# Optimization experiments

Hardware: AMD Instinct MI355X
Metric: run time of the kernel (lower is better)

Reference implementation:

```python
import jax, jax.numpy as jnp
import numpy as np

B, C, IMG, P, E, H, F, L, NC = 32, 1, 224, 16, 256, 16, 3072, 12, 8
NP_ = (IMG // P) ** 2          # 196 patches
S = NP_ + 1                    # 197 tokens (cls + patches)
HD = E // H                    # 16 head dim
DVL, DVR, DVT = NP_ // 4 + 1, NP_ // 4, NP_ // 4   # 50, 49, 49 -> sum + DVT = 197


def _ln(x, g, b, eps=1e-5):
    m = x.mean(-1, keepdims=True)
    v = ((x - m) ** 2).mean(-1, keepdims=True)
    return (x - m) / jnp.sqrt(v + eps) * g + b


def setup_inputs():
    key = jax.random.key(0)
    ks = iter(jax.random.split(key, 64))
    def w(shape, s=0.02):
        return jax.random.normal(next(ks), shape, jnp.float32) * s
    return dict(
        x=jax.random.normal(next(ks), (B, C, IMG, IMG), jnp.float32),
        W_patch=w((E, C, P, P)), b_patch=jnp.zeros((E,), jnp.float32),
        cls_tok=w((1, 1, E), 1.0), pos_emb=w((1, S, E), 1.0),
        Wkl=w((E, E)), bkl=jnp.zeros((E,), jnp.float32),
        Wvl=w((DVL, E)), bvl=jnp.zeros((DVL,), jnp.float32),
        Wkr=w((E, E)), bkr=jnp.zeros((E,), jnp.float32),
        Wvr=w((DVR, E)), bvr=jnp.zeros((DVR,), jnp.float32),
        Wkt=w((E, E)), bkt=jnp.zeros((E,), jnp.float32),
        Wvt=w((DVT, E)), bvt=jnp.zeros((DVT,), jnp.float32),
        ln1_g=jnp.ones((L, E), jnp.float32), ln1_b=jnp.zeros((L, E), jnp.float32),
        Wqkv=w((L, 3 * E, E)), bqkv=jnp.zeros((L, 3 * E), jnp.float32),
        Wo=w((L, E, E)), bo=jnp.zeros((L, E), jnp.float32),
        ln2_g=jnp.ones((L, E), jnp.float32), ln2_b=jnp.zeros((L, E), jnp.float32),
        W1=w((L, F, E)), b1=jnp.zeros((L, F), jnp.float32),
        W2=w((L, E, F)), b2=jnp.zeros((L, E), jnp.float32),
        lnf_g=jnp.ones((E,), jnp.float32), lnf_b=jnp.zeros((E,), jnp.float32),
        W_head=w((NC, E)), b_head=jnp.zeros((NC,), jnp.float32),
    )


def reference(x, W_patch, b_patch, cls_tok, pos_emb,
              Wkl, bkl, Wvl, bvl, Wkr, bkr, Wvr, bvr, Wkt, bkt, Wvt, bvt,
              ln1_g, ln1_b, Wqkv, bqkv, Wo, bo, ln2_g, ln2_b, W1, b1, W2, b2,
              lnf_g, lnf_b, W_head, b_head):
    Bsz = x.shape[0]
    scale_k = 1.0 / jnp.sqrt(jnp.float32(E))
    # patch embedding: conv with stride == kernel == patch size
    h = jax.lax.conv_general_dilated(x, W_patch, (P, P), 'VALID',
                                     dimension_numbers=('NCHW', 'OIHW', 'NCHW'))
    h = h + b_patch[None, :, None, None]                   # (B, E, 14, 14)
    h = h.reshape(Bsz, E, NP_).transpose(0, 2, 1)          # (B, 196, E)
    h = jnp.concatenate([jnp.broadcast_to(cls_tok, (Bsz, 1, E)), h], 1) + pos_emb

    # linear rotatory attention fusing each sample with its batch neighbors
    def rag(xl, xt, xr):                                   # each (S, E)
        rt = xt.mean(0)                                    # target summary (E,)
        al = jax.nn.softmax((xl @ Wkl.T + bkl) @ rt * scale_k)
        rl = al @ (xl @ Wvl.T + bvl)                       # (DVL,)
        ar = jax.nn.softmax((xr @ Wkr.T + bkr) @ rt * scale_k)
        rr = ar @ (xr @ Wvr.T + bvr)                       # (DVR,)
        kt = xt @ Wkt.T + bkt
        vt = xt @ Wvt.T + bvt
        rtl = jax.nn.softmax(kt @ xl.mean(0) * scale_k) @ vt   # (DVT,)
        rtr = jax.nn.softmax(kt @ xr.mean(0) * scale_k) @ vt   # (DVT,)
        f = jnp.concatenate([rl, rtl, rtr, rr])            # (S,) = 50+49+49+49
        return jnp.outer(f, rt)                            # (S, E)

    mid = jax.vmap(rag)(h[:-2], h[1:-1], h[2:])            # (B-2, S, E) batched (no per-sample loop)
    h = jnp.concatenate([h[:1], mid, h[-1:]], 0)

    # standard pre-LN transformer encoder, scanned over stacked layer params
    def block(carry, p):
        g1, b1n, wqkv, bq, wo, bo_, g2, b2n, w1, bb1, w2, bb2 = p
        xn = _ln(carry, g1, b1n)
        qkv = xn @ wqkv.T + bq                             # (B, S, 3E)
        q, k, v = jnp.split(qkv, 3, axis=-1)
        q = q.reshape(Bsz, S, H, HD)
        k = k.reshape(Bsz, S, H, HD)
        v = v.reshape(Bsz, S, H, HD)
        att = jnp.einsum('bqhd,bkhd->bhqk', q, k) / jnp.sqrt(jnp.float32(HD))
        att = jax.nn.softmax(att, axis=-1)
        o = jnp.einsum('bhqk,bkhd->bqhd', att, v).reshape(Bsz, S, E)
        carry = carry + o @ wo.T + bo_
        xn2 = _ln(carry, g2, b2n)
        ff = jax.nn.gelu(xn2 @ w1.T + bb1, approximate=False) @ w2.T + bb2
        return carry + ff, None

    h, _ = jax.lax.scan(block, h, (ln1_g, ln1_b, Wqkv, bqkv, Wo, bo,
                                   ln2_g, ln2_b, W1, b1, W2, b2))
    cls = _ln(h[:, 0], lnf_g, lnf_b)
    return cls @ W_head.T + b_head
```

## Files before the change

kernel.cpp:

```cpp
#include <hip/hip_runtime.h>
#include <hip/hip_bf16.h>
#include <math.h>

constexpr int Bz  = 32;
constexpr int S   = 197;
constexpr int E   = 256;
constexpr int Hn  = 16;
constexpr int HD  = 16;
constexpr int Fd  = 3072;
constexpr int Ln  = 12;
constexpr int MS  = Bz * S;
constexpr int MP  = 6400;
constexpr int NPAT = 6272;
constexpr int DVL = 50, DVR = 49, DVT = 49;
constexpr size_t WLSTRIDE = 1835008;

typedef __attribute__((ext_vector_type(8))) short short8;
typedef __attribute__((ext_vector_type(4))) short short4v;
typedef __attribute__((ext_vector_type(4))) float f32x4;

__device__ __forceinline__ unsigned short f2bf(float f) {
    unsigned int u = __float_as_uint(f);
    u = (u + 0x7FFFu + ((u >> 16) & 1u)) >> 16;
    return (unsigned short)u;
}

__device__ __forceinline__ void gload_lds16(const void* g, void* l) {
    __builtin_amdgcn_global_load_lds(
        (const __attribute__((address_space(1))) void*)g,
        (__attribute__((address_space(3))) void*)l, 16, 0, 0);
}

__device__ __forceinline__ float wave_reduce(float v, int op) {
    #pragma unroll
    for (int off = 32; off > 0; off >>= 1) {
        float o = __shfl_xor(v, off, 64);
        v = op ? fmaxf(v, o) : v + o;
    }
    return v;
}

__device__ __forceinline__ float block_reduce(float v, float* red4, int op) {
    v = wave_reduce(v, op);
    int w = threadIdx.x >> 6;
    if ((threadIdx.x & 63) == 0) red4[w] = v;
    __syncthreads();
    float r = op ? fmaxf(fmaxf(red4[0], red4[1]), fmaxf(red4[2], red4[3]))
                 : (red4[0] + red4[1] + red4[2] + red4[3]);
    __syncthreads();
    return r;
}

__global__ __launch_bounds__(256) void patchify_kernel(
        const float* __restrict__ x, unsigned short* __restrict__ Ab) {
    int pi = blockIdx.x;
    int b = pi / 196, q = pi % 196;
    int i = q / 14, j = q % 14;
    int e = threadIdx.x, pr = e >> 4, pc = e & 15;
    float v = x[((size_t)(b * 224 + i * 16 + pr)) * 224 + j * 16 + pc];
    Ab[(size_t)pi * 256 + e] = f2bf(v);
}

__global__ __launch_bounds__(256) void cls_pos_kernel(
        const float* __restrict__ cls, const float* __restrict__ pos,
        float* __restrict__ h0) {
    int b = blockIdx.x, e = threadIdx.x;
    h0[(size_t)(b * S) * E + e] = cls[e] + pos[e];
}

__global__ __launch_bounds__(256) void convert_kernel(
        const float* __restrict__ src, unsigned short* __restrict__ dst) {
    int i4 = (blockIdx.x * 256 + threadIdx.x) * 4;
    float4 v = *(const float4*)(src + i4);
    ushort4 o;
    o.x = f2bf(v.x); o.y = f2bf(v.y); o.z = f2bf(v.z); o.w = f2bf(v.w);
    *(ushort4*)(dst + i4) = o;
}

__global__ __launch_bounds__(256) void convert_w_all_kernel(
        const float* __restrict__ wqkv, const float* __restrict__ wo,
        const float* __restrict__ w1, const float* __restrict__ w2,
        unsigned short* __restrict__ out) {
    size_t idx = (size_t)blockIdx.x * 256 + threadIdx.x;
    int l = (int)(idx / 458752);
    int r4 = (int)(idx % 458752) * 4;
    const float* src;
    if (r4 < 196608)       src = wqkv + (size_t)l * 196608 + r4;
    else if (r4 < 262144)  src = wo   + (size_t)l * 65536  + (r4 - 196608);
    else if (r4 < 1048576) src = w1   + (size_t)l * 786432 + (r4 - 262144);
    else                   src = w2   + (size_t)l * 786432 + (r4 - 1048576);
    float4 v = *(const float4*)src;
    ushort4 o;
    o.x = f2bf(v.x); o.y = f2bf(v.y); o.z = f2bf(v.z); o.w = f2bf(v.w);
    *(ushort4*)(out + (size_t)l * WLSTRIDE + r4) = o;
}

__global__ __launch_bounds__(256) void means_kernel(
        const float* __restrict__ h0, float* __restrict__ M) {
    int b = blockIdx.x, e = threadIdx.x;
    float s = 0.f;
    for (int t = 0; t < S; t++) s += h0[((size_t)(b * S + t)) * E + e];
    M[b * E + e] = s * (1.f / (float)S);
}

__global__ __launch_bounds__(256) void uvec_kernel(
        const float* __restrict__ M,
        const float* __restrict__ Wkl, const float* __restrict__ bkl,
        const float* __restrict__ Wkr, const float* __restrict__ bkr,
        const float* __restrict__ Wkt, const float* __restrict__ bkt,
        float* __restrict__ Ul, float* __restrict__ Ur, float* __restrict__ Ut,
        float* __restrict__ cl, float* __restrict__ cr, float* __restrict__ ct) {
    __shared__ float red4[4];
    int t = blockIdx.x, e = threadIdx.x;
    const float* mt = M + t * E;
    float a0 = 0.f, a1 = 0.f, a2 = 0.f;
    for (int i = 0; i < 256; i++) {
        float mi = mt[i];
        a0 += Wkl[(size_t)i * 256 + e] * mi;
        a1 += Wkr[(size_t)i * 256 + e] * mi;
        a2 += Wkt[(size_t)i * 256 + e] * mi;
    }
    Ul[t * E + e] = a0; Ur[t * E + e] = a1; Ut[t * E + e] = a2;
    float me = mt[e];
    float c0 = block_reduce(bkl[e] * me, red4, 0);
    float c1 = block_reduce(bkr[e] * me, red4, 0);
    float c2 = block_reduce(bkt[e] * me, red4, 0);
    if (e == 0) { cl[t] = c0; cr[t] = c1; ct[t] = c2; }
}

__global__ __launch_bounds__(256) void rag_score_kernel(
        const float* __restrict__ h0, const float* __restrict__ M,
        const float* __restrict__ Ul, const float* __restrict__ Ur,
        const float* __restrict__ Ut,
        const float* __restrict__ cl, const float* __restrict__ cr,
        const float* __restrict__ ct,
        const float* __restrict__ Wvl, const float* __restrict__ bvl,
        const float* __restrict__ Wvr, const float* __restrict__ bvr,
        const float* __restrict__ Wvt, const float* __restrict__ bvt,
        float* __restrict__ fbuf) {
    int t = blockIdx.x >> 2, br = blockIdx.x & 3;
    const float* xsrc; const float* u; float c;
    const float* Wv; const float* bv; int dv, fo;
    if (br == 0)      { xsrc = h0 + (size_t)t * S * E;       u = Ul + (t+1)*E; c = cl[t+1]; Wv = Wvl; bv = bvl; dv = DVL; fo = 0; }
    else if (br == 1) { xsrc = h0 + (size_t)(t+1) * S * E;   u = Ut + t*E;     c = ct[t];   Wv = Wvt; bv = bvt; dv = DVT; fo = DVL; }
    else if (br == 2) { xsrc = h0 + (size_t)(t+1) * S * E;   u = Ut + (t+2)*E; c = ct[t+2]; Wv = Wvt; bv = bvt; dv = DVT; fo = DVL + DVT; }
    else              { xsrc = h0 + (size_t)(t+2) * S * E;   u = Ur + (t+1)*E; c = cr[t+1]; Wv = Wvr; bv = bvr; dv = DVR; fo = DVL + 2*DVT; }
    __shared__ float us[256], sc[200], xbar[256], red4[4];
    int tid = threadIdx.x, w = tid >> 6, lane = tid & 63;
    us[tid] = u[tid];
    __syncthreads();
    float4 u4 = *(float4*)&us[lane * 4];
    for (int s = w; s < S; s += 4) {
        float4 x4 = *(const float4*)&xsrc[(size_t)s * E + lane * 4];
        float p = x4.x*u4.x + x4.y*u4.y + x4.z*u4.z + x4.w*u4.w;
        p = wave_reduce(p, 0);
        if (lane == 0) sc[s] = (p + c) * 0.0625f;
    }
    __syncthreads();
    float v = (tid < S) ? sc[tid] : -1e30f;
    float mx = block_reduce(v, red4, 1);
    float ex = (tid < S) ? expf(v - mx) : 0.f;
    float dn = block_reduce(ex, red4, 0);
    if (tid < S) sc[tid] = ex / dn;
    __syncthreads();
    float xb = 0.f;
    for (int s = 0; s < S; s++) xb += sc[s] * xsrc[(size_t)s * E + tid];
    xbar[tid] = xb;
    __syncthreads();
    float4 xb4 = *(float4*)&xbar[lane * 4];
    for (int d = w; d < dv; d += 4) {
        float4 w4 = *(const float4*)&Wv[(size_t)d * E + lane * 4];
        float p = w4.x*xb4.x + w4.y*xb4.y + w4.z*xb4.z + w4.w*xb4.w;
        p = wave_reduce(p, 0);
        if (lane == 0) fbuf[t * 256 + fo + d] = p + bv[d];
    }
}

__global__ __launch_bounds__(256) void rag_outer_kernel(
        const float* __restrict__ fbuf, const float* __restrict__ M,
        float* __restrict__ h1) {
    int bid = blockIdx.x;
    int t = bid / S, s = bid % S;
    float f = fbuf[t * 256 + s];
    int e = threadIdx.x;
    h1[((size_t)((t + 1) * S + s)) * E + e] = f * M[(t + 1) * E + e];
}

__global__ __launch_bounds__(256) void copy_edges(const float* __restrict__ h0,
                                                  float* __restrict__ h1) {
    int i = blockIdx.x * 256 + threadIdx.x;
    int n = S * E;
    if (i < n) h1[i] = h0[i];
    else if (i < 2 * n) {
        int j = i - n;
        size_t o = (size_t)31 * S * E + j;
        h1[o] = h0[o];
    }
}

__global__ __launch_bounds__(256) void ln_kernel(const float* __restrict__ in,
                                                 unsigned short* __restrict__ out,
                                                 const float* __restrict__ g,
                                                 const float* __restrict__ b) {
    int w = threadIdx.x >> 6, lane = threadIdx.x & 63;
    int tok = blockIdx.x * 4 + w;
    const float* row = in + (size_t)tok * E;
    float4 v = *(const float4*)&row[lane * 4];
    float mean = wave_reduce(v.x + v.y + v.z + v.w, 0) * (1.f / 256.f);
    float dx = v.x - mean, dy = v.y - mean, dz = v.z - mean, dw = v.w - mean;
    float var = wave_reduce(dx*dx + dy*dy + dz*dz + dw*dw, 0) * (1.f / 256.f);
    float inv = rsqrtf(var + 1e-5f);
    float4 gg = *(const float4*)&g[lane * 4];
    float4 bb = *(const float4*)&b[lane * 4];
    ushort4 o;
    o.x = f2bf(dx * inv * gg.x + bb.x);
    o.y = f2bf(dy * inv * gg.y + bb.y);
    o.z = f2bf(dz * inv * gg.z + bb.z);
    o.w = f2bf(dw * inv * gg.w + bb.w);
    *(ushort4*)&out[(size_t)tok * E + lane * 4] = o;
}

template <int MODE>
__global__ __launch_bounds__(256) void gemm_s64(
        const unsigned short* __restrict__ A, int lda,
        const unsigned short* __restrict__ W, int ldw,
        const float* __restrict__ bias,
        void* __restrict__ Cv, int ldc, int K, int MT, int NT,
        const float* __restrict__ pos) {
    __shared__ unsigned short As[2 * 64 * 64];
    __shared__ unsigned short Bs[2 * 64 * 64];
    const int id = blockIdx.x;
    const int mt = (id & 7) + 8 * (id / (8 * NT));
    const int nt = (id >> 3) % NT;
    if (mt >= MT) return;
    const int m0 = mt * 64, n0 = nt * 64;
    const int tid = threadIdx.x, wave = tid >> 6, lane = tid & 63;
    const int lr = lane & 15, kg = lane >> 4;
    const int srow = wave * 16 + (lane >> 3);
    const int scol = ((lane & 7) ^ (lane >> 3)) * 8;
    auto stage = [&](int bb, int k0) {
        #pragma unroll
        for (int q = 0; q < 2; q++) {
            gload_lds16(&A[(size_t)(m0 + srow + q * 8) * lda + k0 + scol],
                        &As[bb * 4096 + (wave * 16 + q * 8) * 64]);
            gload_lds16(&W[(size_t)(n0 + srow + q * 8) * ldw + k0 + scol],
                        &Bs[bb * 4096 + (wave * 16 + q * 8) * 64]);
        }
    };
    const int nIter = K >> 6;
    stage(0, 0);
    f32x4 acc[4] = {};
    for (int i = 0; i < nIter; i++) {
        __syncthreads();
        if (i + 1 < nIter) stage((i + 1) & 1, (i + 1) * 64);
        const int bb = i & 1;
        #pragma unroll
        for (int h = 0; h < 2; h++) {
            const int sw = ((h * 4 + kg) ^ (lr & 7)) * 8;
            short8 af = *(short8*)&As[bb * 4096 + (wave * 16 + lr) * 64 + sw];
            #pragma unroll
            for (int j = 0; j < 4; j++) {
                short8 bf = *(short8*)&Bs[bb * 4096 + (j * 16 + lr) * 64 + sw];
                acc[j] = __builtin_amdgcn_mfma_f32_16x16x32_bf16(af, bf, acc[j], 0, 0, 0);
            }
        }
    }
    #pragma unroll
    for (int j = 0; j < 4; j++) {
        int n = n0 + j * 16 + lr;
        float bv = bias ? bias[n] : 0.f;
        #pragma unroll
        for (int r = 0; r < 4; r++) {
            int m = m0 + wave * 16 + kg * 4 + r;
            float v = acc[j][r] + bv;
            if (MODE == 1) ((float*)Cv)[(size_t)m * ldc + n] += v;
            if (MODE == 2) {
                v = 0.5f * v * (1.f + erff(v * 0.70710678118654752f));
                ((unsigned short*)Cv)[(size_t)m * ldc + n] = f2bf(v);
            }
            if (MODE == 3) {
                int b = m / 196, s = m - b * 196 + 1;
                ((float*)Cv)[((size_t)(b * S + s)) * E + n] = v + pos[(size_t)s * E + n];
            }
            if (MODE == 4) ((unsigned short*)Cv)[(size_t)m * ldc + n] = f2bf(v);
        }
    }
}

static inline int s64_grid(int MT, int NT) { return ((MT + 7) / 8) * 8 * NT; }

__global__ __launch_bounds__(256) void attn_kernel(
        const unsigned short* __restrict__ qkv, unsigned short* __restrict__ o) {
    int b = blockIdx.x >> 4, hh = blockIdx.x & 15;
    __shared__ unsigned short Qs[208][32];
    __shared__ unsigned short Ks[208][32];
    __shared__ unsigned short Vt[16][224];
    __shared__ unsigned short Ps[4][16][224];
    int tid = threadIdx.x, wave = tid >> 6, lane = tid & 63;
    int lr = lane & 15, kg = lane >> 4;
    short8 z8 = {};
    if (tid < 208) {
        if (tid < 197) {
            size_t row = (size_t)(b * S + tid) * 768 + hh * 16;
            *(short8*)&Qs[tid][0] = *(const short8*)&qkv[row];
            *(short8*)&Qs[tid][8] = *(const short8*)&qkv[row + 8];
            *(short8*)&Ks[tid][0] = *(const short8*)&qkv[row + 256];
            *(short8*)&Ks[tid][8] = *(const short8*)&qkv[row + 264];
            union { short8 v8[2]; unsigned short u[16]; } vv;
            vv.v8[0] = *(const short8*)&qkv[row + 512];
            vv.v8[1] = *(const short8*)&qkv[row + 520];
            #pragma unroll
            for (int d = 0; d < 16; d++) Vt[d][tid] = vv.u[d];
        } else {
            *(short8*)&Qs[tid][0] = z8; *(short8*)&Qs[tid][8] = z8;
            *(short8*)&Ks[tid][0] = z8; *(short8*)&Ks[tid][8] = z8;
            #pragma unroll
            for (int d = 0; d < 16; d++) Vt[d][tid] = 0;
        }
        *(short8*)&Qs[tid][16] = z8; *(short8*)&Qs[tid][24] = z8;
        *(short8*)&Ks[tid][16] = z8; *(short8*)&Ks[tid][24] = z8;
    } else if (tid < 224) {
        #pragma unroll
        for (int d = 0; d < 16; d++) Vt[d][tid] = 0;
    }
    {
        short4v z4 = {};
        *(short4v*)&Ps[wave][lane >> 2][208 + (lane & 3) * 4] = z4;
    }
    __syncthreads();
    const f32x4 zf = {0.f, 0.f, 0.f, 0.f};
    for (int it = wave; it < 13; it += 4) {
        short8 qa = *(short8*)&Qs[it * 16 + lr][kg * 8];
        f32x4 sc[13];
        #pragma unroll
        for (int j = 0; j < 13; j++) {
            short8 kb = *(short8*)&Ks[j * 16 + lr][kg * 8];
            sc[j] = __builtin_amdgcn_mfma_f32_16x16x32_bf16(qa, kb, zf, 0, 0, 0);
        }
        float m[4] = {-1e30f, -1e30f, -1e30f, -1e30f};
        #pragma unroll
        for (int j = 0; j < 13; j++) {
            if (j * 16 + lr < 197) {
                #pragma unroll
                for (int r = 0; r < 4; r++) m[r] = fmaxf(m[r], sc[j][r]);
            }
        }
        #pragma unroll
        for (int off = 1; off < 16; off <<= 1)
            #pragma unroll
            for (int r = 0; r < 4; r++) m[r] = fmaxf(m[r], __shfl_xor(m[r], off, 64));
        float l[4] = {0.f, 0.f, 0.f, 0.f};
        #pragma unroll
        for (int j = 0; j < 13; j++) {
            bool valid = (j * 16 + lr) < 197;
            #pragma unroll
            for (int r = 0; r < 4; r++) {
                float p = valid ? __expf((sc[j][r] - m[r]) * 0.25f) : 0.f;
                l[r] += p;
                Ps[wave][kg * 4 + r][j * 16 + lr] = f2bf(p);
            }
        }
        #pragma unroll
        for (int off = 1; off < 16; off <<= 1)
            #pragma unroll
            for (int r = 0; r < 4; r++) l[r] += __shfl_xor(l[r], off, 64);
        f32x4 oa = zf;
        #pragma unroll
        for (int k0 = 0; k0 < 224; k0 += 32) {
            short8 pa = *(short8*)&Ps[wave][lr][k0 + kg * 8];
            short8 vb = *(short8*)&Vt[lr][k0 + kg * 8];
            oa = __builtin_amdgcn_mfma_f32_16x16x32_bf16(pa, vb, oa, 0, 0, 0);
        }
        #pragma unroll
        for (int r = 0; r < 4; r++) {
            int q = it * 16 + kg * 4 + r;
            if (q < 197)
                o[((size_t)(b * S + q)) * 256 + hh * 16 + lr] = f2bf(oa[r] / l[r]);
        }
    }
}

__global__ __launch_bounds__(256) void head_kernel(
        const float* __restrict__ h, const float* __restrict__ g,
        const float* __restrict__ bb, const float* __restrict__ Wh,
        const float* __restrict__ bh, float* __restrict__ out) {
    __shared__ float red4[4];
    __shared__ float xs[256];
    int b = blockIdx.x, e = threadIdx.x;
    float v = h[((size_t)(b * S)) * E + e];
    float mean = block_reduce(v, red4, 0) * (1.f / 256.f);
    float d = v - mean;
    float var = block_reduce(d * d, red4, 0) * (1.f / 256.f);
    float xn = d * rsqrtf(var + 1e-5f) * g[e] + bb[e];
    xs[e] = xn;
    __syncthreads();
    for (int n = 0; n < 8; n++) {
        float s = block_reduce(xs[e] * Wh[(size_t)n * 256 + e], red4, 0);
        if (e == 0) out[b * 8 + n] = s + bh[n];
    }
}

extern "C" void kernel_launch(void* const* d_in, const int* in_sizes, int n_in,
                              void* d_out, int out_size, void* d_ws, size_t ws_size,
                              hipStream_t stream) {
    const float* x      = (const float*)d_in[0];
    const float* W_patch= (const float*)d_in[1];
    const float* b_patch= (const float*)d_in[2];
    const float* cls_tok= (const float*)d_in[3];
    const float* pos_emb= (const float*)d_in[4];
    const float* Wkl = (const float*)d_in[5];   const float* bkl = (const float*)d_in[6];
    const float* Wvl = (const float*)d_in[7];   const float* bvl = (const float*)d_in[8];
    const float* Wkr = (const float*)d_in[9];   const float* bkr = (const float*)d_in[10];
    const float* Wvr = (const float*)d_in[11];  const float* bvr = (const float*)d_in[12];
    const float* Wkt = (const float*)d_in[13];  const float* bkt = (const float*)d_in[14];
    const float* Wvt = (const float*)d_in[15];  const float* bvt = (const float*)d_in[16];
    const float* ln1_g = (const float*)d_in[17]; const float* ln1_b = (const float*)d_in[18];
    const float* Wqkv  = (const float*)d_in[19]; const float* bqkv  = (const float*)d_in[20];
    const float* Wo    = (const float*)d_in[21]; const float* bo    = (const float*)d_in[22];
    const float* ln2_g = (const float*)d_in[23]; const float* ln2_b = (const float*)d_in[24];
    const float* W1 = (const float*)d_in[25];   const float* b1 = (const float*)d_in[26];
    const float* W2 = (const float*)d_in[27];   const float* b2 = (const float*)d_in[28];
    const float* lnf_g = (const float*)d_in[29]; const float* lnf_b = (const float*)d_in[30];
    const float* W_head = (const float*)d_in[31]; const float* b_head = (const float*)d_in[32];

    char* p = (char*)d_ws;
    unsigned short* regionB = (unsigned short*)p; p += (size_t)MP * 1536 * 2;
    float* h1 = (float*)p;                        p += (size_t)MP * 256 * 4;
    unsigned short* xnb = (unsigned short*)p;     p += (size_t)MP * 256 * 2;
    unsigned short* wall = (unsigned short*)p;
    unsigned short* qkb = regionB;
    unsigned short* ob  = regionB + 5242880;
    unsigned short* ff  = regionB;
    float* h0 = (float*)regionB;
    unsigned short* wp_b = ob;
    float* ragws = (float*)((char*)regionB + 7340032);
    float* M    = ragws;
    float* Ul   = ragws + 8192;
    float* Ur   = ragws + 2 * 8192;
    float* Ut   = ragws + 3 * 8192;
    float* cl   = ragws + 4 * 8192;
    float* cr   = cl + 32;
    float* ct   = cl + 64;
    float* fbuf = cl + 96;

    convert_w_all_kernel<<<21504, 256, 0, stream>>>(Wqkv, Wo, W1, W2, wall);

    convert_kernel<<<128, 256, 0, stream>>>(W_patch, wp_b);
    patchify_kernel<<<NPAT, 256, 0, stream>>>(x, xnb);
    cls_pos_kernel<<<Bz, 256, 0, stream>>>(cls_tok, pos_emb, h0);
    gemm_s64<3><<<s64_grid(98, 4), 256, 0, stream>>>(
        xnb, 256, wp_b, 256, b_patch, h0, 256, 256, 98, 4, pos_emb);

    means_kernel<<<Bz, 256, 0, stream>>>(h0, M);
    uvec_kernel<<<Bz, 256, 0, stream>>>(M, Wkl, bkl, Wkr, bkr, Wkt, bkt,
                                        Ul, Ur, Ut, cl, cr, ct);
    rag_score_kernel<<<(Bz - 2) * 4, 256, 0, stream>>>(
        h0, M, Ul, Ur, Ut, cl, cr, ct, Wvl, bvl, Wvr, bvr, Wvt, bvt, fbuf);
    rag_outer_kernel<<<(Bz - 2) * S, 256, 0, stream>>>(fbuf, M, h1);
    copy_edges<<<(2 * S * E + 255) / 256, 256, 0, stream>>>(h0, h1);

    for (int l = 0; l < Ln; l++) {
        const unsigned short* wqkv_b = wall + (size_t)l * WLSTRIDE;
        const unsigned short* wo_b   = wqkv_b + 196608;
        const unsigned short* w1_b   = wqkv_b + 262144;
        const unsigned short* w2_b   = wqkv_b + 1048576;
        ln_kernel<<<MS / 4, 256, 0, stream>>>(h1, xnb, ln1_g + l * E, ln1_b + l * E);
        gemm_s64<4><<<s64_grid(100, 12), 256, 0, stream>>>(
            xnb, 256, wqkv_b, 256, bqkv + l * 768, qkb, 768, 256, 100, 12, nullptr);
        attn_kernel<<<Bz * Hn, 256, 0, stream>>>(qkb, ob);
        gemm_s64<1><<<s64_grid(100, 4), 256, 0, stream>>>(
            ob, 256, wo_b, 256, bo + l * 256, h1, 256, 256, 100, 4, nullptr);
        ln_kernel<<<MS / 4, 256, 0, stream>>>(h1, xnb, ln2_g + l * E, ln2_b + l * E);
        for (int c = 0; c < 2; c++) {
            gemm_s64<2><<<s64_grid(100, 24), 256, 0, stream>>>(
                xnb, 256, w1_b + (size_t)c * 1536 * 256, 256, b1 + l * Fd + c * 1536,
                ff, 1536, 256, 100, 24, nullptr);
            gemm_s64<1><<<s64_grid(100, 4), 256, 0, stream>>>(
                ff, 1536, w2_b + c * 1536, 3072, (c == 0 ? b2 + l * 256 : nullptr),
                h1, 256, 1536, 100, 4, nullptr);
        }
    }
    head_kernel<<<Bz, 256, 0, stream>>>(h1, lnf_g, lnf_b, W_head, b_head, (float*)d_out);
}
```

Before: 1.748 ms.

## Use 128x128 tile GEMM for FFN up-projection and unsplit FFN, vectorize RAG reductions

Adds a gemm_s128 kernel with 128x128 tiles and a 4x4 MFMA accumulator per wave, used for the W1+GELU projection over the full 3072 width. The FFN is no longer split into two 1536-wide chunks, which removes extra launches and one read-modify-write pass over h1 per layer. To make room, the workspace is reorganized into separate, non-aliased buffers, including a full 6400x3072 bf16 FFN buffer. The small RAG prologue kernels (means, uvec, weighted sum) switch to float4 loads with a per-wave split and shared-memory reduction. The costs are more workspace memory and higher register pressure in the larger tile.

After: 1.661 ms. 1.05x faster.

```diff
diff --git a/kernel.cpp b/kernel.cpp
--- a/kernel.cpp
+++ b/kernel.cpp
@@ -97,10 +97,17 @@
 
 __global__ __launch_bounds__(256) void means_kernel(
         const float* __restrict__ h0, float* __restrict__ M) {
-    int b = blockIdx.x, e = threadIdx.x;
-    float s = 0.f;
-    for (int t = 0; t < S; t++) s += h0[((size_t)(b * S + t)) * E + e];
-    M[b * E + e] = s * (1.f / (float)S);
+    __shared__ float part[4][256];
+    int b = blockIdx.x, tid = threadIdx.x, w = tid >> 6, lane = tid & 63;
+    float4 a = {0.f, 0.f, 0.f, 0.f};
+    for (int t = w; t < S; t += 4) {
+        float4 v = *(const float4*)&h0[((size_t)(b * S + t)) * E + lane * 4];
+        a.x += v.x; a.y += v.y; a.z += v.z; a.w += v.w;
+    }
+    *(float4*)&part[w][lane * 4] = a;
+    __syncthreads();
+    M[b * E + tid] = (part[0][tid] + part[1][tid] + part[2][tid] + part[3][tid])
+                     * (1.f / (float)S);
 }
 
 __global__ __launch_bounds__(256) void uvec_kernel(
@@ -110,22 +117,31 @@
         const float* __restrict__ Wkt, const float* __restrict__ bkt,
         float* __restrict__ Ul, float* __restrict__ Ur, float* __restrict__ Ut,
         float* __restrict__ cl, float* __restrict__ cr, float* __restrict__ ct) {
-    __shared__ float red4[4];
-    int t = blockIdx.x, e = threadIdx.x;
+    __shared__ float p0[4][256], p1[4][256], p2[4][256], red4[4];
+    int t = blockIdx.x, tid = threadIdx.x, w = tid >> 6, lane = tid & 63;
     const float* mt = M + t * E;
-    float a0 = 0.f, a1 = 0.f, a2 = 0.f;
-    for (int i = 0; i < 256; i++) {
+    float4 a0 = {0,0,0,0}, a1 = {0,0,0,0}, a2 = {0,0,0,0};
+    for (int i = w * 64; i < w * 64 + 64; i++) {
         float mi = mt[i];
-        a0 += Wkl[(size_t)i * 256 + e] * mi;
-        a1 += Wkr[(size_t)i * 256 + e] * mi;
-        a2 += Wkt[(size_t)i * 256 + e] * mi;
-    }
-    Ul[t * E + e] = a0; Ur[t * E + e] = a1; Ut[t * E + e] = a2;
-    float me = mt[e];
-    float c0 = block_reduce(bkl[e] * me, red4, 0);
-    float c1 = block_reduce(bkr[e] * me, red4, 0);
-    float c2 = block_reduce(bkt[e] * me, red4, 0);
-    if (e == 0) { cl[t] = c0; cr[t] = c1; ct[t] = c2; }
+        float4 v0 = *(const float4*)&Wkl[(size_t)i * 256 + lane * 4];
+        float4 v1 = *(const float4*)&Wkr[(size_t)i * 256 + lane * 4];
+        float4 v2 = *(const float4*)&Wkt[(size_t)i * 256 + lane * 4];
+        a0.x += v0.x * mi; a0.y += v0.y * mi; a0.z += v0.z * mi; a0.w += v0.w * mi;
+        a1.x += v1.x * mi; a1.y += v1.y * mi; a1.z += v1.z * mi; a1.w += v1.w * mi;
+        a2.x += v2.x * mi; a2.y += v2.y * mi; a2.z += v2.z * mi; a2.w += v2.w * mi;
+    }
+    *(float4*)&p0[w][lane * 4] = a0;
+    *(float4*)&p1[w][lane * 4] = a1;
+    *(float4*)&p2[w][lane * 4] = a2;
+    __syncthreads();
+    Ul[t * E + tid] = p0[0][tid] + p0[1][tid] + p0[2][tid] + p0[3][tid];
+    Ur[t * E + tid] = p1[0][tid] + p1[1][tid] + p1[2][tid] + p1[3][tid];
+    Ut[t * E + tid] = p2[0][tid] + p2[1][tid] + p2[2][tid] + p2[3][tid];
+    float me = mt[tid];
+    float c0 = block_reduce(bkl[tid] * me, red4, 0);
+    float c1 = block_reduce(bkr[tid] * me, red4, 0);
+    float c2 = block_reduce(bkt[tid] * me, red4, 0);
+    if (tid == 0) { cl[t] = c0; cr[t] = c1; ct[t] = c2; }
 }
 
 __global__ __launch_bounds__(256) void rag_score_kernel(
@@ -145,7 +161,7 @@
     else if (br == 1) { xsrc = h0 + (size_t)(t+1) * S * E;   u = Ut + t*E;     c = ct[t];   Wv = Wvt; bv = bvt; dv = DVT; fo = DVL; }
     else if (br == 2) { xsrc = h0 + (size_t)(t+1) * S * E;   u = Ut + (t+2)*E; c = ct[t+2]; Wv = Wvt; bv = bvt; dv = DVT; fo = DVL + DVT; }
     else              { xsrc = h0 + (size_t)(t+2) * S * E;   u = Ur + (t+1)*E; c = cr[t+1]; Wv = Wvr; bv = bvr; dv = DVR; fo = DVL + 2*DVT; }
-    __shared__ float us[256], sc[200], xbar[256], red4[4];
+    __shared__ float us[256], sc[200], xbar[256], part[4][256], red4[4];
     int tid = threadIdx.x, w = tid >> 6, lane = tid & 63;
     us[tid] = u[tid];
     __syncthreads();
@@ -163,9 +179,15 @@
     float dn = block_reduce(ex, red4, 0);
     if (tid < S) sc[tid] = ex / dn;
     __syncthreads();
-    float xb = 0.f;
-    for (int s = 0; s < S; s++) xb += sc[s] * xsrc[(size_t)s * E + tid];
-    xbar[tid] = xb;
+    float4 pa = {0.f, 0.f, 0.f, 0.f};
+    for (int s = w; s < S; s += 4) {
+        float a = sc[s];
+        float4 x4 = *(const float4*)&xsrc[(size_t)s * E + lane * 4];
+        pa.x += a * x4.x; pa.y += a * x4.y; pa.z += a * x4.z; pa.w += a * x4.w;
+    }
+    *(float4*)&part[w][lane * 4] = pa;
+    __syncthreads();
+    xbar[tid] = part[0][tid] + part[1][tid] + part[2][tid] + part[3][tid];
     __syncthreads();
     float4 xb4 = *(float4*)&xbar[lane * 4];
     for (int d = w; d < dv; d += 4) {
@@ -274,10 +296,6 @@
             int m = m0 + wave * 16 + kg * 4 + r;
             float v = acc[j][r] + bv;
             if (MODE == 1) ((float*)Cv)[(size_t)m * ldc + n] += v;
-            if (MODE == 2) {
-                v = 0.5f * v * (1.f + erff(v * 0.70710678118654752f));
-                ((unsigned short*)Cv)[(size_t)m * ldc + n] = f2bf(v);
-            }
             if (MODE == 3) {
                 int b = m / 196, s = m - b * 196 + 1;
                 ((float*)Cv)[((size_t)(b * S + s)) * E + n] = v + pos[(size_t)s * E + n];
@@ -287,7 +305,75 @@
     }
 }
 
-static inline int s64_grid(int MT, int NT) { return ((MT + 7) / 8) * 8 * NT; }
+template <int MODE>
+__global__ __launch_bounds__(256) void gemm_s128(
+        const unsigned short* __restrict__ A, int lda,
+        const unsigned short* __restrict__ W, int ldw,
+        const float* __restrict__ bias,
+        void* __restrict__ Cv, int ldc, int K, int MT, int NT) {
+    __shared__ unsigned short As[2 * 128 * 64];
+    __shared__ unsigned short Bs[2 * 128 * 64];
+    const int id = blockIdx.x;
+    const int mt = (id & 7) + 8 * (id / (8 * NT));
+    const int nt = (id >> 3) % NT;
+    if (mt >= MT) return;
+    const int m0 = mt * 128, n0 = nt * 128;
+    const int tid = threadIdx.x, wave = tid >> 6, lane = tid & 63;
+    const int wm = (wave >> 1) * 64, wn = (wave & 1) * 64;
+    const int lr = lane & 15, kg = lane >> 4;
+    const int srow = wave * 32 + (lane >> 3);
+    const int scol = ((lane & 7) ^ (lane >> 3)) * 8;
+    auto stage = [&](int bb, int k0) {
+        #pragma unroll
+        for (int q = 0; q < 4; q++) {
+            gload_lds16(&A[(size_t)(m0 + srow + q * 8) * lda + k0 + scol],
+                        &As[bb * 8192 + (wave * 4 + q) * 512]);
+            gload_lds16(&W[(size_t)(n0 + srow + q * 8) * ldw + k0 + scol],
+                        &Bs[bb * 8192 + (wave * 4 + q) * 512]);
+        }
+    };
+    const int nIter = K >> 6;
+    stage(0, 0);
+    f32x4 acc[4][4] = {};
+    for (int i = 0; i < nIter; i++) {
+        __syncthreads();
+        if (i + 1 < nIter) stage((i + 1) & 1, (i + 1) * 64);
+        const int bb = i & 1;
+        #pragma unroll
+        for (int h = 0; h < 2; h++) {
+            const int sw = ((h * 4 + kg) ^ (lr & 7)) * 8;
+            short8 af[4], bfr[4];
+            #pragma unroll
+            for (int i2 = 0; i2 < 4; i2++) af[i2]  = *(short8*)&As[bb * 8192 + (wm + i2 * 16 + lr) * 64 + sw];
+            #pragma unroll
+            for (int j = 0; j < 4; j++) bfr[j] = *(short8*)&Bs[bb * 8192 + (wn + j * 16 + lr) * 64 + sw];
+            #pragma unroll
+            for (int i2 = 0; i2 < 4; i2++)
+                #pragma unroll
+                for (int j = 0; j < 4; j++)
+                    acc[i2][j] = __builtin_amdgcn_mfma_f32_16x16x32_bf16(af[i2], bfr[j], acc[i2][j], 0, 0, 0);
+        }
+    }
+    #pragma unroll
+    for (int j = 0; j < 4; j++) {
+        int n = n0 + wn + j * 16 + lr;
+        float bv = bias ? bias[n] : 0.f;
+        #pragma unroll
+        for (int i = 0; i < 4; i++) {
+            #pragma unroll
+            for (int r = 0; r < 4; r++) {
+                size_t m = (size_t)(m0 + wm + i * 16 + kg * 4 + r);
+                float v = acc[i][j][r] + bv;
+                if (MODE == 2) {
+                    v = 0.5f * v * (1.f + erff(v * 0.70710678118654752f));
+                    ((unsigned short*)Cv)[m * ldc + n] = f2bf(v);
+                }
+            }
+        }
+    }
+}
+
+static inline int sg(int MT, int NT) { return ((MT + 7) / 8) * 8 * NT; }
 
 __global__ __launch_bounds__(256) void attn_kernel(
         const unsigned short* __restrict__ qkv, unsigned short* __restrict__ o) {
@@ -424,16 +510,15 @@
     const float* W_head = (const float*)d_in[31]; const float* b_head = (const float*)d_in[32];
 
     char* p = (char*)d_ws;
-    unsigned short* regionB = (unsigned short*)p; p += (size_t)MP * 1536 * 2;
-    float* h1 = (float*)p;                        p += (size_t)MP * 256 * 4;
-    unsigned short* xnb = (unsigned short*)p;     p += (size_t)MP * 256 * 2;
+    float* h0 = (float*)p;                    p += (size_t)MP * 256 * 4;
+    float* h1 = (float*)p;                    p += (size_t)MP * 256 * 4;
+    unsigned short* qkb = (unsigned short*)p; p += (size_t)MP * 768 * 2;
+    unsigned short* xnb = (unsigned short*)p; p += (size_t)MP * 256 * 2;
+    unsigned short* ob  = (unsigned short*)p; p += (size_t)MP * 256 * 2;
+    unsigned short* ff  = (unsigned short*)p; p += (size_t)MP * 3072 * 2;
+    unsigned short* wpb = (unsigned short*)p; p += (size_t)65536 * 2;
+    float* ragws = (float*)p;                 p += (size_t)40960 * 4;
     unsigned short* wall = (unsigned short*)p;
-    unsigned short* qkb = regionB;
-    unsigned short* ob  = regionB + 5242880;
-    unsigned short* ff  = regionB;
-    float* h0 = (float*)regionB;
-    unsigned short* wp_b = ob;
-    float* ragws = (float*)((char*)regionB + 7340032);
     float* M    = ragws;
     float* Ul   = ragws + 8192;
     float* Ur   = ragws + 2 * 8192;
@@ -445,11 +530,11 @@
 
     convert_w_all_kernel<<<21504, 256, 0, stream>>>(Wqkv, Wo, W1, W2, wall);
 
-    convert_kernel<<<128, 256, 0, stream>>>(W_patch, wp_b);
+    convert_kernel<<<64, 256, 0, stream>>>(W_patch, wpb);
     patchify_kernel<<<NPAT, 256, 0, stream>>>(x, xnb);
     cls_pos_kernel<<<Bz, 256, 0, stream>>>(cls_tok, pos_emb, h0);
-    gemm_s64<3><<<s64_grid(98, 4), 256, 0, stream>>>(
-        xnb, 256, wp_b, 256, b_patch, h0, 256, 256, 98, 4, pos_emb);
+    gemm_s64<3><<<sg(98, 4), 256, 0, stream>>>(
+        xnb, 256, wpb, 256, b_patch, h0, 256, 256, 98, 4, pos_emb);
 
     means_kernel<<<Bz, 256, 0, stream>>>(h0, M);
     uvec_kernel<<<Bz, 256, 0, stream>>>(M, Wkl, bkl, Wkr, bkr, Wkt, bkt,
@@ -465,20 +550,16 @@
         const unsigned short* w1_b   = wqkv_b + 262144;
         const unsigned short* w2_b   = wqkv_b + 1048576;
         ln_kernel<<<MS / 4, 256, 0, stream>>>(h1, xnb, ln1_g + l * E, ln1_b + l * E);
-        gemm_s64<4><<<s64_grid(100, 12), 256, 0, stream>>>(
+        gemm_s64<4><<<sg(100, 12), 256, 0, stream>>>(
             xnb, 256, wqkv_b, 256, bqkv + l * 768, qkb, 768, 256, 100, 12, nullptr);
         attn_kernel<<<Bz * Hn, 256, 0, stream>>>(qkb, ob);
-        gemm_s64<1><<<s64_grid(100, 4), 256, 0, stream>>>(
+        gemm_s64<1><<<sg(100, 4), 256, 0, stream>>>(
             ob, 256, wo_b, 256, bo + l * 256, h1, 256, 256, 100, 4, nullptr);
         ln_kernel<<<MS / 4, 256, 0, stream>>>(h1, xnb, ln2_g + l * E, ln2_b + l * E);
-        for (int c = 0; c < 2; c++) {
-            gemm_s64<2><<<s64_grid(100, 24), 256, 0, stream>>>(
-                xnb, 256, w1_b + (size_t)c * 1536 * 256, 256, b1 + l * Fd + c * 1536,
-                ff, 1536, 256, 100, 24, nullptr);
-            gemm_s64<1><<<s64_grid(100, 4), 256, 0, stream>>>(
-                ff, 1536, w2_b + c * 1536, 3072, (c == 0 ? b2 + l * 256 : nullptr),
-                h1, 256, 1536, 100, 4, nullptr);
-        }
+        gemm_s128<2><<<sg(50, 24), 256, 0, stream>>>(
+            xnb, 256, w1_b, 256, b1 + l * Fd, ff, 3072, 256, 50, 24);
+        gemm_s64<1><<<sg(100, 4), 256, 0, stream>>>(
+            ff, 3072, w2_b, 3072, b2 + l * 256, h1, 256, 3072, 100, 4, nullptr);
     }
     head_kernel<<<Bz, 256, 0, stream>>>(h1, lnf_g, lnf_b, W_head, b_head, (float*)d_out);
 }
```
